# Kernel tuning notes

Measured on AMD Instinct MI355X. Metric: run time of the kernel, lower is better.

Reference implementation:

```python
import jax, jax.numpy as jnp
import numpy as np

N_CLASSES = 4
N_STEPS = 10
THRESHOLD = 0.7
ALPHA = 2.0


def _make_kernel_bias(n_classes, threshold):
    cross = np.zeros((3, 3, 3), dtype=np.float32)
    cross[1, 1, :] = 1.0
    cross[1, :, 1] = 1.0
    cross[:, 1, 1] = 1.0
    # depthwise kernel, OIDHW with I = 1 (groups = n_classes)
    kernel = (1.0 / 7.0 / (1.0 - threshold)) * np.tile(cross[None, None], (n_classes, 1, 1, 1, 1))
    bias = np.full((n_classes,), -threshold / (1.0 - threshold), dtype=np.float32)
    return jnp.asarray(kernel), jnp.asarray(bias)


def setup_inputs() -> dict:
    key = jax.random.key(0)
    k1, k2, k3 = jax.random.split(key, 3)
    B, C, D, H, W = 2, N_CLASSES, 128, 128, 128
    inp = jax.random.normal(k1, (B, C, D, H, W), dtype=jnp.float32)
    target = jax.random.randint(k2, (B, D, H, W), 0, C, dtype=jnp.int64)
    weight = jax.random.uniform(k3, (B, C), dtype=jnp.float32)
    kernel, bias = _make_kernel_bias(C, THRESHOLD)
    return {"input": inp, "target": target, "weight": weight, "kernel": kernel, "bias": bias}


def _erode(op, kernel, bias, n_classes):
    y = jax.lax.conv_general_dilated(
        op, kernel, window_strides=(1, 1, 1), padding=[(1, 1)] * 3,
        dimension_numbers=("NCDHW", "OIDHW", "NCDHW"),
        feature_group_count=n_classes)
    return jnp.maximum(y + bias[None, :, None, None, None], 0.0)


def reference(input, target, weight, kernel, bias):
    C = N_CLASSES
    probs = jax.nn.softmax(input, axis=1)
    # one_hot -> [B, D, H, W, C] -> [B, C, D, H, W]
    tgt = jnp.transpose(jax.nn.one_hot(target, C, dtype=probs.dtype), (0, 4, 1, 2, 3))
    op = jnp.square(probs - tgt)
    loss_t = jnp.zeros_like(op)
    for k in range(N_STEPS):
        op = _erode(op, kernel, bias, C)
        loss_t = loss_t + (float(k + 1) ** ALPHA) * op
    loss_t = loss_t * weight[:, :, None, None, None]
    return jnp.mean(loss_t)
```

## Files before the change

kernel.cpp:

```cpp
#include <hip/hip_runtime.h>

#define DHW   (128*128*128)
#define CDHW  (4*DHW)
#define NTOT  (2*CDHW)
#define NACC  1024

#define ROW4     32
#define IN_ROWS  12
#define S1_ROWS  10
#define IN_P4    (IN_ROWS*ROW4)
#define S1_P4    (S1_ROWS*ROW4)
#define SLOT4(z) (((z)+8)&3)
#define SLOT2(z) (((z)+8)&1)


__global__ __launch_bounds__(256, 4) void fused_sm_erode2_kernel(
    const float* __restrict__ in, const int* __restrict__ tgt,
    float4* __restrict__ dst,
    const float* __restrict__ kern, const float* __restrict__ bias,
    const float* __restrict__ weight, float c1, float c2,
    double* __restrict__ accs, int* __restrict__ flagOut)
{
    __shared__ float4 lin[4 * IN_P4];
    __shared__ float4 ls1[2 * S1_P4];
    __shared__ double wsum[4];
    __shared__ int    voteArr[16];

    const int tid = threadIdx.x;
    const int x  = blockIdx.x & 7;
    const int q  = blockIdx.x >> 3;
    const int c  = q & 3;
    const int t  = x * 32 + (q >> 2);
    const int y0 = (t & 15) << 3;
    const int zb = ((t >> 4) & 7) << 4;
    const int b  = (t >> 7) & 1;
    const int bc = b * 4 + c;
    const int fid = (bc << 7) | (((t >> 4) & 7) << 4) | (t & 15);

    const float4* in4 = (const float4*)in;
    const int4*   tg4 = (const int4*)tgt;
    const size_t  chb = ((size_t)(b * 4)) << 19;
    const size_t  co0 = chb + ((size_t)c << 19);
    const size_t  co1 = chb + ((size_t)((c + 1) & 3) << 19);
    const size_t  co2 = chb + ((size_t)((c + 2) & 3) << 19);
    const size_t  co3 = chb + ((size_t)((c + 3) & 3) << 19);
    float4*       dp  = dst + ((size_t)bc << 19);
    const float wk = kern[13];
    const float bs = bias[c];

    const int col  = tid & 31;
    const int trow = tid >> 5;

    if (tid < 16) voteArr[tid] = 0;

    const int  gy0  = y0 + trow - 2;
    const bool lv0  = ((unsigned)gy0 < 128u);
    const int  off0 = (lv0 ? gy0 : 0) * 32 + col;
    const bool act1 = (tid < 128);
    const int  gy1  = y0 + trow + 6;
    const bool lv1  = act1 && ((unsigned)gy1 < 128u);
    const int  off1 = (lv1 ? gy1 : 0) * 32 + col;

    const bool  sact1 = (tid < 64);
    const int   sr  = (tid < 32) ? 0 : 9;
    const float m1  = ((unsigned)(y0 + sr - 1) < 128u) ? 1.f : 0.f;
    const int   ci1 = (sr + 1) * 32 + (tid & 31);
    const int   so1 = sr * 32 + (tid & 31);

    const float lmask = (col == 0)  ? 0.f : 1.f;
    const float rmask = (col == 31) ? 0.f : 1.f;

    const int go4 = (y0 + trow) * 32 + col;

    const float4 f4z = make_float4(0.f, 0.f, 0.f, 0.f);
    float4 A00 = f4z, A01 = f4z, A02 = f4z, A03 = f4z;
    float4 A10 = f4z, A11 = f4z, A12 = f4z, A13 = f4z;
    int4   T0 = make_int4(0,0,0,0), T1 = make_int4(0,0,0,0);
    bool   ok0 = false, ok1 = false;
    float4 s_m = f4z, s_c = f4z, s_p = f4z;
    float4 vH  = f4z;

    auto prefetch = [&](int L) {
        const bool zok = ((unsigned)L < 128u);
        ok0 = zok && lv0;
        ok1 = zok && lv1;
        if (ok0) {
            size_t o = (size_t)(L << 12) + off0;
            A00 = in4[co0 + o];
            A01 = in4[co1 + o];
            A02 = in4[co2 + o];
            A03 = in4[co3 + o];
            T0  = tg4[((size_t)b << 19) + o];
        }
        if (ok1) {
            size_t o = (size_t)(L << 12) + off1;
            A10 = in4[co0 + o];
            A11 = in4[co1 + o];
            A12 = in4[co2 + o];
            A13 = in4[co3 + o];
            T1  = tg4[((size_t)b << 19) + o];
        }
    };
    auto op_one = [&](const float4& B0, const float4& B1, const float4& B2,
                      const float4& B3, const int4& T) -> float4 {
        float4 r;
        #define OP1(K)                                                         \
        {                                                                      \
            float vc = B0.K;                                                   \
            float sm = 1.0f + __expf(B1.K - vc) + __expf(B2.K - vc)            \
                            + __expf(B3.K - vc);                               \
            float d  = __builtin_amdgcn_rcpf(sm) - ((T.K == c) ? 1.0f : 0.0f); \
            r.K = d * d;                                                       \
        }
        OP1(x) OP1(y) OP1(z) OP1(w)
        #undef OP1
        return r;
    };
    auto commit = [&](int L) {
        float4* sl = lin + SLOT4(L) * IN_P4;
        float4 v0 = f4z, v1 = f4z;
        if (ok0) v0 = op_one(A00, A01, A02, A03, T0);
        if (ok1) v1 = op_one(A10, A11, A12, A13, T1);
        sl[tid] = v0;
        if (act1) sl[256 + tid] = v1;
    };
    auto s1one = [&](const float4* pzm, const float4* pzc, const float4* pzp,
                     int ci, float ym) -> float4 {
        float4 qC = pzc[ci];
        float4 qU = pzc[ci - 32];
        float4 qD = pzc[ci + 32];
        float4 qm = pzm[ci];
        float4 qp = pzp[ci];
        float lf = __shfl_up(qC.w, 1, 64)   * lmask;
        float rt = __shfl_down(qC.x, 1, 64) * rmask;
        float4 v;
        v.x = fmaxf((qC.x + lf   + qC.y + qU.x + qD.x + qm.x + qp.x) * wk + bs, 0.f) * ym;
        v.y = fmaxf((qC.y + qC.x + qC.z + qU.y + qD.y + qm.y + qp.y) * wk + bs, 0.f) * ym;
        v.z = fmaxf((qC.z + qC.y + qC.w + qU.z + qD.z + qm.z + qp.z) * wk + bs, 0.f) * ym;
        v.w = fmaxf((qC.w + qC.z + rt   + qU.w + qD.w + qm.w + qp.w) * wk + bs, 0.f) * ym;
        return v;
    };
    auto s1_phase = [&](int z) {
        float4* o = ls1 + SLOT2(z) * S1_P4;
        float4 vnew;
        if ((unsigned)z < 128u) {
            const float4* pzm = lin + SLOT4(z - 1) * IN_P4;
            const float4* pzc = lin + SLOT4(z)     * IN_P4;
            const float4* pzp = lin + SLOT4(z + 1) * IN_P4;
            vnew = s1one(pzm, pzc, pzp, tid + 64, 1.f);
            o[tid + 32] = vnew;
            if (sact1) o[so1] = s1one(pzm, pzc, pzp, ci1, m1);
        } else {
            vnew = f4z;
            o[tid + 32] = f4z;
            if (sact1) o[so1] = f4z;
        }
        s_m = s_c; s_c = s_p; s_p = vnew;
    };

    double part = 0.0;

    prefetch(zb - 2); commit(zb - 2);
    prefetch(zb - 1); commit(zb - 1);
    prefetch(zb);     commit(zb);
    prefetch(zb + 1);
    __syncthreads();
    s1_phase(zb - 1);

    for (int L = zb + 1; L <= zb + 17; ++L) {
        commit(L);
        __syncthreads();
        const int zp = L - 3;
        if (zp >= zb && voteArr[zp - zb] != 0)
            dp[((size_t)zp << 12) + go4] = vH;
        if (L <= zb + 16) prefetch(L + 1);
        s1_phase(L - 1);
        const int zo = L - 2;
        if (zo >= zb) {
            const float4* su = ls1 + SLOT2(zo) * S1_P4;
            float4 u4 = su[tid];
            float4 d4 = su[tid + 64];
            float lf = __shfl_up(s_c.w, 1, 64)   * lmask;
            float rt = __shfl_down(s_c.x, 1, 64) * rmask;
            float4 v;
            v.x = fmaxf((s_c.x + lf    + s_c.y + u4.x + d4.x + s_m.x + s_p.x) * wk + bs, 0.f);
            v.y = fmaxf((s_c.y + s_c.x + s_c.z + u4.y + d4.y + s_m.y + s_p.y) * wk + bs, 0.f);
            v.z = fmaxf((s_c.z + s_c.y + s_c.w + u4.z + d4.z + s_m.z + s_p.z) * wk + bs, 0.f);
            v.w = fmaxf((s_c.w + s_c.z + rt    + u4.w + d4.w + s_m.w + s_p.w) * wk + bs, 0.f);
            float pl = c1 * (s_c.x + s_c.y + s_c.z + s_c.w)
                     + c2 * (v.x   + v.y   + v.z   + v.w);
            part += (double)pl;
            bool nzv = (v.x != 0.f) || (v.y != 0.f) || (v.z != 0.f) || (v.w != 0.f);
            if (__any(nzv) && (tid & 63) == 0) atomicOr(&voteArr[zo - zb], 1);
            vH = v;
        }
    }

    __syncthreads();
    if (voteArr[15] != 0) dp[((size_t)(zb + 15) << 12) + go4] = vH;

    #pragma unroll
    for (int off = 32; off > 0; off >>= 1)
        part += __shfl_down(part, off, 64);
    if ((tid & 63) == 0) wsum[tid >> 6] = part;
    __syncthreads();
    if (tid == 0) {
        int mask = 0;
        #pragma unroll
        for (int i = 0; i < 16; ++i) mask |= (voteArr[i] ? 1 : 0) << i;
        flagOut[fid] = mask;
        double tot = (wsum[0] + wsum[1] + wsum[2] + wsum[3]) * (double)weight[bc];
        accs[blockIdx.x] = tot;
    }
}

#define E4_INP4  512
#define E4_S1P4  448
#define E4_S2P4  384
#define E4_S3P4  320

__global__ __launch_bounds__(256, 2) void erode4_kernel(
    const float4* __restrict__ src, float4* __restrict__ dst,
    const float* __restrict__ kern, const float* __restrict__ bias,
    const float* __restrict__ weight,
    float c1, float c2, float c3, float c4,
    int store, double* __restrict__ accs,
    const int* __restrict__ flagIn, int* __restrict__ flagOut)
{
    __shared__ float4 lin[4 * E4_INP4];
    __shared__ float4 ls1[2 * E4_S1P4];
    __shared__ float4 ls2[2 * E4_S2P4];
    __shared__ float4 ls3[2 * E4_S3P4];
    __shared__ double wsum[4];
    __shared__ int    sf[9];
    __shared__ int    voteArr[16];
    __shared__ unsigned sAIn;

    const int tid = threadIdx.x;
    const int bid = ((blockIdx.x & 7) << 7) | (blockIdx.x >> 3);
    const int ty = bid & 15;
    const int tz = (bid >> 4) & 7;
    const int y0 = ty << 3;
    const int zb = tz << 4;
    const int bc = bid >> 7;

    if (tid < 9) {
        int dy = tid % 3 - 1, dz = tid / 3 - 1;
        int yt = ty + dy, zt = tz + dz;
        int f = 0;
        if ((unsigned)yt < 16u && (unsigned)zt < 8u)
            f = flagIn[(bc << 7) | (zt << 4) | yt];
        sf[tid] = f;
    }
    __syncthreads();

    bool abit = false;
    if (tid < 24) {
        int L = zb - 4 + tid;
        if ((unsigned)L < 128u) {
            int zi = (L >> 4) - tz + 1;
            int m  = sf[zi * 3] | sf[zi * 3 + 1] | sf[zi * 3 + 2];
            abit = (m >> (L & 15)) & 1;
        }
    }
    unsigned long long bal = __ballot(abit);
    if (tid == 0) sAIn = (unsigned)bal;
    __syncthreads();
    const unsigned aIn = sAIn;
    if (aIn == 0) { if (tid == 0) flagOut[bid] = 0; return; }

    unsigned zc = 0xFFFFFFu;
    if (zb == 0)   zc &= 0xFFFFF0u;
    if (zb == 112) zc &= 0x0FFFFFu;
    const unsigned a1 = (aIn | aIn << 1 | aIn >> 1) & zc & 0x7FFFFEu;
    const unsigned a2 = (a1  | a1  << 1 | a1  >> 1) & zc & 0x3FFFFCu;
    const unsigned a3 = (a2  | a2  << 1 | a2  >> 1) & zc & 0x1FFFF8u;
    const unsigned a4 = (a3  | a3  << 1 | a3  >> 1) & zc & 0x0FFFF0u;

    if (tid < 16) voteArr[tid] = 0;

    const int fa  = __builtin_ctz(aIn);
    const int la  = 31 - __builtin_clz(aIn);
    const int loL = zb - 4 + (fa > 2 ? fa - 2 : 0);
    const int hiL = zb - 4 + (la + 8 < 23 ? la + 8 : 23);

    const float4* sp = src + ((size_t)bc << 19);
    float4*       dp = dst + ((size_t)bc << 19);
    const float wk = kern[13];
    const float bs = bias[bc & 3];

    const int col  = tid & 31;
    const int trow = tid >> 5;
    const int g    = trow;

    const int  gy0 = y0 - 4 + trow;
    const int  gy1 = y0 + 4 + trow;
    const bool lv0 = ((unsigned)gy0 < 128u);
    const bool lv1 = ((unsigned)gy1 < 128u);
    const int  off0 = (lv0 ? gy0 : 0) * 32 + col;
    const int  off1 = (lv1 ? gy1 : 0) * 32 + col;
    const int  yd0 = ((unsigned)((gy0 >> 3) - ty + 1) < 3u) ? ((gy0 >> 3) - ty + 1) : 1;
    const int  yd1 = ((unsigned)((gy1 >> 3) - ty + 1) < 3u) ? ((gy1 >> 3) - ty + 1) : 1;

    const int   r1  = (g < 3) ? g : g + 8;
    const float ym1 = ((unsigned)(y0 - 3 + r1) < 128u) ? 1.f : 0.f;
    const int   ci1 = (r1 + 1) * 32 + col;
    const int   R2  = (g < 2) ? g : g + 8;
    const float ym2 = ((unsigned)(y0 - 2 + R2) < 128u) ? 1.f : 0.f;
    const int   ci2 = (R2 + 2) * 32 + col;
    const int   S3  = g * 9;
    const float ym3 = ((unsigned)(y0 - 1 + S3) < 128u) ? 1.f : 0.f;
    const int   ci3 = (S3 + 3) * 32 + col;

    const float lmask = (col == 0)  ? 0.f : 1.f;
    const float rmask = (col == 31) ? 0.f : 1.f;
    const int   go4  = (y0 + trow) * 32 + col;

    const float4 f4z = make_float4(0.f, 0.f, 0.f, 0.f);
    float4 pf0 = f4z, pf1 = f4z;
    float4 p1m=f4z,p1c=f4z,p1p=f4z;
    float4 p2m=f4z,p2c=f4z,p2p=f4z;
    float4 p3m=f4z,p3c=f4z,p3p=f4z;
    float4 o1m=f4z,o1c=f4z,o1p=f4z;
    float4 q1m=f4z,q1c=f4z,q1p=f4z;
    float4 q2m=f4z,q2c=f4z,q2p=f4z;
    float4 vH = f4z;
    double part = 0.0;

    auto st7 = [&](const float4& zm, const float4& cc, const float4& zp,
                   const float4& u, const float4& d, float ym) -> float4 {
        float lf = __shfl_up(cc.w, 1, 64)   * lmask;
        float rt = __shfl_down(cc.x, 1, 64) * rmask;
        float4 v;
        v.x = fmaxf((cc.x + lf   + cc.y + u.x + d.x + zm.x + zp.x) * wk + bs, 0.f) * ym;
        v.y = fmaxf((cc.y + cc.x + cc.z + u.y + d.y + zm.y + zp.y) * wk + bs, 0.f) * ym;
        v.z = fmaxf((cc.z + cc.y + cc.w + u.z + d.z + zm.z + zp.z) * wk + bs, 0.f) * ym;
        v.w = fmaxf((cc.w + cc.z + rt   + u.w + d.w + zm.w + zp.w) * wk + bs, 0.f) * ym;
        return v;
    };
    auto s1at = [&](int z, int ci, float ym) -> float4 {
        const float4* pzm = lin + SLOT4(z - 1) * E4_INP4;
        const float4* pzc = lin + SLOT4(z)     * E4_INP4;
        const float4* pzp = lin + SLOT4(z + 1) * E4_INP4;
        return st7(pzm[ci], pzc[ci], pzp[ci], pzc[ci - 32], pzc[ci + 32], ym);
    };
    auto prefetch = [&](int L) {
        pf0 = f4z; pf1 = f4z;
        if (L >= zb - 4 && L <= zb + 19 && (unsigned)L < 128u) {
            const int zi = (L >> 4) - tz + 1;
            const int sh = L & 15;
            const float4* zp = sp + ((size_t)L << 12);
            if (lv0 && ((sf[zi * 3 + yd0] >> sh) & 1)) pf0 = zp[off0];
            if (lv1 && ((sf[zi * 3 + yd1] >> sh) & 1)) pf1 = zp[off1];
        }
    };
    auto commit = [&](int L) {
        float4* sl = lin + SLOT4(L) * E4_INP4;
        sl[trow * 32 + col]       = pf0;
        sl[(trow + 8) * 32 + col] = pf1;
    };

    prefetch(loL);
    for (int L = loL; L <= hiL; ++L) {
        commit(L);
        __syncthreads();
        const int zs = L - 5;
        if (store && zs >= zb && voteArr[zs - zb] != 0)
            dp[((size_t)zs << 12) + go4] = vH;
        if (L < hiL) prefetch(L + 1);

        {
            const int z = L - 1, ib = z - (zb - 4);
            float4 vp = f4z, vo = f4z, vq = f4z;
            if ((unsigned)ib < 24u && ((a1 >> ib) & 1)) {
                vp = s1at(z, (trow + 4) * 32 + col, 1.f);
                float4* o = ls1 + SLOT2(z) * E4_S1P4;
                if (tid < 192) o[r1 * 32 + col] = s1at(z, ci1, ym1);
                if (tid < 128) vo = s1at(z, ci2, ym2);
                if (tid < 64)  vq = s1at(z, ci3, ym3);
                o[(trow + 3) * 32 + col] = vp;
                if (z >= zb && z <= zb + 15)
                    part += (double)(c1 * (vp.x + vp.y + vp.z + vp.w));
            }
            p1m = p1c; p1c = p1p; p1p = vp;
            o1m = o1c; o1c = o1p; o1p = vo;
            q1m = q1c; q1c = q1p; q1p = vq;
        }
        {
            const int z = L - 2, ib = z - (zb - 4);
            float4 vp = f4z, vq = f4z;
            if ((unsigned)ib < 24u && ((a2 >> ib) & 1)) {
                const bool l1 = ((a1 >> ib) & 1);
                const float4* s1p_ = ls1 + SLOT2(z) * E4_S1P4;
                float4 u = l1 ? s1p_[(trow + 2) * 32 + col] : f4z;
                float4 d = l1 ? s1p_[(trow + 4) * 32 + col] : f4z;
                vp = st7(p1m, p1c, p1p, u, d, 1.f);
                float4* o = ls2 + SLOT2(z) * E4_S2P4;
                if (tid < 128) {
                    float4 u2 = l1 ? s1p_[R2 * 32 + col]       : f4z;
                    float4 d2 = l1 ? s1p_[(R2 + 2) * 32 + col] : f4z;
                    o[R2 * 32 + col] = st7(o1m, o1c, o1p, u2, d2, ym2);
                }
                if (tid < 64) {
                    float4 u3 = l1 ? s1p_[(S3 + 1) * 32 + col] : f4z;
                    float4 d3 = l1 ? s1p_[(S3 + 3) * 32 + col] : f4z;
                    vq = st7(q1m, q1c, q1p, u3, d3, ym3);
                }
                o[(trow + 2) * 32 + col] = vp;
                if (z >= zb && z <= zb + 15)
                    part += (double)(c2 * (vp.x + vp.y + vp.z + vp.w));
            }
            p2m = p2c; p2c = p2p; p2p = vp;
            q2m = q2c; q2c = q2p; q2p = vq;
        }
        {
            const int z = L - 3, ib = z - (zb - 4);
            float4 vp = f4z;
            if ((unsigned)ib < 24u && ((a3 >> ib) & 1)) {
                const bool l2 = ((a2 >> ib) & 1);
                const float4* s2p_ = ls2 + SLOT2(z) * E4_S2P4;
                float4 u = l2 ? s2p_[(trow + 1) * 32 + col] : f4z;
                float4 d = l2 ? s2p_[(trow + 3) * 32 + col] : f4z;
                vp = st7(p2m, p2c, p2p, u, d, 1.f);
                float4* o = ls3 + SLOT2(z) * E4_S3P4;
                if (tid < 64) {
                    float4 u3 = l2 ? s2p_[S3 * 32 + col]       : f4z;
                    float4 d3 = l2 ? s2p_[(S3 + 2) * 32 + col] : f4z;
                    o[S3 * 32 + col] = st7(q2m, q2c, q2p, u3, d3, ym3);
                }
                o[(trow + 1) * 32 + col] = vp;
                if (z >= zb && z <= zb + 15)
                    part += (double)(c3 * (vp.x + vp.y + vp.z + vp.w));
            }
            p3m = p3c; p3c = p3p; p3p = vp;
        }
        {
            const int z = L - 4, ib = z - (zb - 4);
            float4 v = f4z;
            if ((unsigned)ib < 24u && ((a4 >> ib) & 1)) {
                const bool l3 = ((a3 >> ib) & 1);
                const float4* s3p_ = ls3 + SLOT2(z) * E4_S3P4;
                float4 u = l3 ? s3p_[trow * 32 + col]       : f4z;
                float4 d = l3 ? s3p_[(trow + 2) * 32 + col] : f4z;
                v = st7(p3m, p3c, p3p, u, d, 1.f);
                part += (double)(c4 * (v.x + v.y + v.z + v.w));
                bool nzv = (v.x != 0.f) || (v.y != 0.f) || (v.z != 0.f) || (v.w != 0.f);
                if (__any(nzv) && (tid & 63) == 0) atomicOr(&voteArr[z - zb], 1);
            }
            vH = v;
        }
    }

    __syncthreads();
    {
        const int hp = hiL - 4;
        if (store && hp >= zb && voteArr[hp - zb] != 0)
            dp[((size_t)hp << 12) + go4] = vH;
    }

    #pragma unroll
    for (int off = 32; off > 0; off >>= 1)
        part += __shfl_down(part, off, 64);
    if ((tid & 63) == 0) wsum[tid >> 6] = part;
    __syncthreads();
    if (tid == 0) {
        int mask = 0;
        #pragma unroll
        for (int i = 0; i < 16; ++i) mask |= (voteArr[i] ? 1 : 0) << i;
        flagOut[bid] = mask;
        double tot = (wsum[0] + wsum[1] + wsum[2] + wsum[3]) * (double)weight[bc];
        atomicAdd(&accs[bid], tot);
    }
}

__global__ __launch_bounds__(1024) void finalize_kernel(
    const double* __restrict__ accs, float* __restrict__ out)
{
    __shared__ double wsum[16];
    double v = accs[threadIdx.x];
    #pragma unroll
    for (int off = 32; off > 0; off >>= 1)
        v += __shfl_down(v, off, 64);
    int lane = threadIdx.x & 63;
    int wid  = threadIdx.x >> 6;
    if (lane == 0) wsum[wid] = v;
    __syncthreads();
    if (threadIdx.x == 0) {
        double tot = 0.0;
        #pragma unroll
        for (int i = 0; i < 16; ++i) tot += wsum[i];
        out[0] = (float)(tot / (double)NTOT);
    }
}

extern "C" void kernel_launch(void* const* d_in, const int* in_sizes, int n_in,
                              void* d_out, int out_size, void* d_ws, size_t ws_size,
                              hipStream_t stream) {
    const float* in     = (const float*)d_in[0];
    const int*   tgt    = (const int*)d_in[1];
    const float* weight = (const float*)d_in[2];
    const float* kern   = (const float*)d_in[3];
    const float* bias   = (const float*)d_in[4];
    float* out = (float*)d_out;

    char* ws = (char*)d_ws;
    float*  buf0   = (float*)ws;
    float*  buf1   = (float*)(ws + (size_t)NTOT * sizeof(float));
    double* accs   = (double*)(ws + (size_t)NTOT * 2 * sizeof(float));
    int*    flagsA = (int*)(ws + (size_t)NTOT * 2 * sizeof(float) + NACC * sizeof(double));
    int*    flagsB = flagsA + NACC;

    fused_sm_erode2_kernel<<<1024, 256, 0, stream>>>(
        in, tgt, (float4*)buf0, kern, bias, weight, 1.0f, 4.0f, accs, flagsA);

    erode4_kernel<<<1024, 256, 0, stream>>>(
        (const float4*)buf0, (float4*)buf1, kern, bias, weight,
        9.0f, 16.0f, 25.0f, 36.0f, 1, accs, flagsA, flagsB);

    erode4_kernel<<<1024, 256, 0, stream>>>(
        (const float4*)buf1, (float4*)buf0, kern, bias, weight,
        49.0f, 64.0f, 81.0f, 100.0f, 0, accs, flagsB, flagsA);

    finalize_kernel<<<1, 1024, 0, stream>>>(accs, out);
}
```

Before: 150.5 us.

## Compact active tiles into a worklist and run persistent erode blocks

Result: slower. 160.5 us (+6.7%).

```diff
diff --git a/kernel.cpp b/kernel.cpp
--- a/kernel.cpp
+++ b/kernel.cpp
@@ -214,6 +214,32 @@
     }
 }
 
+__global__ __launch_bounds__(1024) void wl_build_kernel(
+    const int* __restrict__ flagIn, int* __restrict__ flagOut,
+    int* __restrict__ wl, int* __restrict__ popc)
+{
+    const int t = threadIdx.x;
+    flagOut[t] = 0;
+    if (t == 0) { wl[0] = 0; popc[0] = 0; }
+    __syncthreads();
+
+    const int ty = t & 15, tz = (t >> 4) & 7, bc = t >> 7;
+    int act = 0;
+    #pragma unroll
+    for (int dz = -1; dz <= 1; ++dz) {
+        int zt = tz + dz;
+        if ((unsigned)zt >= 8u) continue;
+        int need = (dz < 0) ? 0xF000 : (dz > 0) ? 0x000F : 0xFFFF;
+        #pragma unroll
+        for (int dy = -1; dy <= 1; ++dy) {
+            int yt = ty + dy;
+            if ((unsigned)yt >= 16u) continue;
+            act |= flagIn[(bc << 7) | (zt << 4) | yt] & need;
+        }
+    }
+    if (act) { int i = atomicAdd(&wl[0], 1); wl[1 + i] = t; }
+}
+
 #define E4_INP4  512
 #define E4_S1P4  448
 #define E4_S2P4  384
@@ -225,7 +251,8 @@
     const float* __restrict__ weight,
     float c1, float c2, float c3, float c4,
     int store, double* __restrict__ accs,
-    const int* __restrict__ flagIn, int* __restrict__ flagOut)
+    const int* __restrict__ flagIn, int* __restrict__ flagOut,
+    const int* __restrict__ wl, int* __restrict__ popc)
 {
     __shared__ float4 lin[4 * E4_INP4];
     __shared__ float4 ls1[2 * E4_S1P4];
@@ -235,241 +262,256 @@
     __shared__ int    sf[9];
     __shared__ int    voteArr[16];
     __shared__ unsigned sAIn;
-
-    const int tid = threadIdx.x;
-    const int bid = ((blockIdx.x & 7) << 7) | (blockIdx.x >> 3);
-    const int ty = bid & 15;
-    const int tz = (bid >> 4) & 7;
-    const int y0 = ty << 3;
-    const int zb = tz << 4;
-    const int bc = bid >> 7;
-
-    if (tid < 9) {
-        int dy = tid % 3 - 1, dz = tid / 3 - 1;
-        int yt = ty + dy, zt = tz + dz;
-        int f = 0;
-        if ((unsigned)yt < 16u && (unsigned)zt < 8u)
-            f = flagIn[(bc << 7) | (zt << 4) | yt];
-        sf[tid] = f;
-    }
-    __syncthreads();
-
-    bool abit = false;
-    if (tid < 24) {
-        int L = zb - 4 + tid;
-        if ((unsigned)L < 128u) {
-            int zi = (L >> 4) - tz + 1;
-            int m  = sf[zi * 3] | sf[zi * 3 + 1] | sf[zi * 3 + 2];
-            abit = (m >> (L & 15)) & 1;
-        }
-    }
-    unsigned long long bal = __ballot(abit);
-    if (tid == 0) sAIn = (unsigned)bal;
-    __syncthreads();
-    const unsigned aIn = sAIn;
-    if (aIn == 0) { if (tid == 0) flagOut[bid] = 0; return; }
-
-    unsigned zc = 0xFFFFFFu;
-    if (zb == 0)   zc &= 0xFFFFF0u;
-    if (zb == 112) zc &= 0x0FFFFFu;
-    const unsigned a1 = (aIn | aIn << 1 | aIn >> 1) & zc & 0x7FFFFEu;
-    const unsigned a2 = (a1  | a1  << 1 | a1  >> 1) & zc & 0x3FFFFCu;
-    const unsigned a3 = (a2  | a2  << 1 | a2  >> 1) & zc & 0x1FFFF8u;
-    const unsigned a4 = (a3  | a3  << 1 | a3  >> 1) & zc & 0x0FFFF0u;
-
-    if (tid < 16) voteArr[tid] = 0;
-
-    const int fa  = __builtin_ctz(aIn);
-    const int la  = 31 - __builtin_clz(aIn);
-    const int loL = zb - 4 + (fa > 2 ? fa - 2 : 0);
-    const int hiL = zb - 4 + (la + 8 < 23 ? la + 8 : 23);
-
-    const float4* sp = src + ((size_t)bc << 19);
-    float4*       dp = dst + ((size_t)bc << 19);
-    const float wk = kern[13];
-    const float bs = bias[bc & 3];
-
+    __shared__ int    sTile;
+
+    const int tid  = threadIdx.x;
+    const int cnt  = wl[0];
     const int col  = tid & 31;
     const int trow = tid >> 5;
     const int g    = trow;
-
-    const int  gy0 = y0 - 4 + trow;
-    const int  gy1 = y0 + 4 + trow;
-    const bool lv0 = ((unsigned)gy0 < 128u);
-    const bool lv1 = ((unsigned)gy1 < 128u);
-    const int  off0 = (lv0 ? gy0 : 0) * 32 + col;
-    const int  off1 = (lv1 ? gy1 : 0) * 32 + col;
-    const int  yd0 = ((unsigned)((gy0 >> 3) - ty + 1) < 3u) ? ((gy0 >> 3) - ty + 1) : 1;
-    const int  yd1 = ((unsigned)((gy1 >> 3) - ty + 1) < 3u) ? ((gy1 >> 3) - ty + 1) : 1;
-
-    const int   r1  = (g < 3) ? g : g + 8;
-    const float ym1 = ((unsigned)(y0 - 3 + r1) < 128u) ? 1.f : 0.f;
-    const int   ci1 = (r1 + 1) * 32 + col;
-    const int   R2  = (g < 2) ? g : g + 8;
-    const float ym2 = ((unsigned)(y0 - 2 + R2) < 128u) ? 1.f : 0.f;
-    const int   ci2 = (R2 + 2) * 32 + col;
-    const int   S3  = g * 9;
-    const float ym3 = ((unsigned)(y0 - 1 + S3) < 128u) ? 1.f : 0.f;
-    const int   ci3 = (S3 + 3) * 32 + col;
-
+    const float wk = kern[13];
     const float lmask = (col == 0)  ? 0.f : 1.f;
     const float rmask = (col == 31) ? 0.f : 1.f;
-    const int   go4  = (y0 + trow) * 32 + col;
-
     const float4 f4z = make_float4(0.f, 0.f, 0.f, 0.f);
-    float4 pf0 = f4z, pf1 = f4z;
-    float4 p1m=f4z,p1c=f4z,p1p=f4z;
-    float4 p2m=f4z,p2c=f4z,p2p=f4z;
-    float4 p3m=f4z,p3c=f4z,p3p=f4z;
-    float4 o1m=f4z,o1c=f4z,o1p=f4z;
-    float4 q1m=f4z,q1c=f4z,q1p=f4z;
-    float4 q2m=f4z,q2c=f4z,q2p=f4z;
-    float4 vH = f4z;
-    double part = 0.0;
-
-    auto st7 = [&](const float4& zm, const float4& cc, const float4& zp,
-                   const float4& u, const float4& d, float ym) -> float4 {
-        float lf = __shfl_up(cc.w, 1, 64)   * lmask;
-        float rt = __shfl_down(cc.x, 1, 64) * rmask;
-        float4 v;
-        v.x = fmaxf((cc.x + lf   + cc.y + u.x + d.x + zm.x + zp.x) * wk + bs, 0.f) * ym;
-        v.y = fmaxf((cc.y + cc.x + cc.z + u.y + d.y + zm.y + zp.y) * wk + bs, 0.f) * ym;
-        v.z = fmaxf((cc.z + cc.y + cc.w + u.z + d.z + zm.z + zp.z) * wk + bs, 0.f) * ym;
-        v.w = fmaxf((cc.w + cc.z + rt   + u.w + d.w + zm.w + zp.w) * wk + bs, 0.f) * ym;
-        return v;
-    };
-    auto s1at = [&](int z, int ci, float ym) -> float4 {
-        const float4* pzm = lin + SLOT4(z - 1) * E4_INP4;
-        const float4* pzc = lin + SLOT4(z)     * E4_INP4;
-        const float4* pzp = lin + SLOT4(z + 1) * E4_INP4;
-        return st7(pzm[ci], pzc[ci], pzp[ci], pzc[ci - 32], pzc[ci + 32], ym);
-    };
-    auto prefetch = [&](int L) {
-        pf0 = f4z; pf1 = f4z;
-        if (L >= zb - 4 && L <= zb + 19 && (unsigned)L < 128u) {
-            const int zi = (L >> 4) - tz + 1;
-            const int sh = L & 15;
-            const float4* zp = sp + ((size_t)L << 12);
-            if (lv0 && ((sf[zi * 3 + yd0] >> sh) & 1)) pf0 = zp[off0];
-            if (lv1 && ((sf[zi * 3 + yd1] >> sh) & 1)) pf1 = zp[off1];
-        }
-    };
-    auto commit = [&](int L) {
-        float4* sl = lin + SLOT4(L) * E4_INP4;
-        sl[trow * 32 + col]       = pf0;
-        sl[(trow + 8) * 32 + col] = pf1;
-    };
-
-    prefetch(loL);
-    for (int L = loL; L <= hiL; ++L) {
-        commit(L);
-        __syncthreads();
-        const int zs = L - 5;
-        if (store && zs >= zb && voteArr[zs - zb] != 0)
-            dp[((size_t)zs << 12) + go4] = vH;
-        if (L < hiL) prefetch(L + 1);
-
+
+    for (;;) {
+        if (tid == 0) {
+            int i = atomicAdd(popc, 1);
+            sTile = (i < cnt) ? wl[1 + i] : -1;
+        }
+        __syncthreads();
+        const int tile = sTile;
+        __syncthreads();
+        if (tile < 0) break;
+
+        const int ty = tile & 15;
+        const int tz = (tile >> 4) & 7;
+        const int y0 = ty << 3;
+        const int zb = tz << 4;
+        const int bc = tile >> 7;
+
+        if (tid < 9) {
+            int dy = tid % 3 - 1, dz = tid / 3 - 1;
+            int yt = ty + dy, zt = tz + dz;
+            int f = 0;
+            if ((unsigned)yt < 16u && (unsigned)zt < 8u)
+                f = flagIn[(bc << 7) | (zt << 4) | yt];
+            sf[tid] = f;
+        }
+        __syncthreads();
+
+        bool abit = false;
+        if (tid < 24) {
+            int L = zb - 4 + tid;
+            if ((unsigned)L < 128u) {
+                int zi = (L >> 4) - tz + 1;
+                int m  = sf[zi * 3] | sf[zi * 3 + 1] | sf[zi * 3 + 2];
+                abit = (m >> (L & 15)) & 1;
+            }
+        }
+        unsigned long long bal = __ballot(abit);
+        if (tid == 0) sAIn = (unsigned)bal;
+        __syncthreads();
+        const unsigned aIn = sAIn;
+        if (aIn == 0) continue;
+
+        unsigned zc = 0xFFFFFFu;
+        if (zb == 0)   zc &= 0xFFFFF0u;
+        if (zb == 112) zc &= 0x0FFFFFu;
+        const unsigned a1 = (aIn | aIn << 1 | aIn >> 1) & zc & 0x7FFFFEu;
+        const unsigned a2 = (a1  | a1  << 1 | a1  >> 1) & zc & 0x3FFFFCu;
+        const unsigned a3 = (a2  | a2  << 1 | a2  >> 1) & zc & 0x1FFFF8u;
+        const unsigned a4 = (a3  | a3  << 1 | a3  >> 1) & zc & 0x0FFFF0u;
+
+        if (tid < 16) voteArr[tid] = 0;
+
+        const int fa  = __builtin_ctz(aIn);
+        const int la  = 31 - __builtin_clz(aIn);
+        const int loL = zb - 4 + (fa > 2 ? fa - 2 : 0);
+        const int hiL = zb - 4 + (la + 8 < 23 ? la + 8 : 23);
+
+        const float4* sp = src + ((size_t)bc << 19);
+        float4*       dp = dst + ((size_t)bc << 19);
+        const float bs = bias[bc & 3];
+
+        const int  gy0 = y0 - 4 + trow;
+        const int  gy1 = y0 + 4 + trow;
+        const bool lv0 = ((unsigned)gy0 < 128u);
+        const bool lv1 = ((unsigned)gy1 < 128u);
+        const int  off0 = (lv0 ? gy0 : 0) * 32 + col;
+        const int  off1 = (lv1 ? gy1 : 0) * 32 + col;
+        const int  yd0 = ((unsigned)((gy0 >> 3) - ty + 1) < 3u) ? ((gy0 >> 3) - ty + 1) : 1;
+        const int  yd1 = ((unsigned)((gy1 >> 3) - ty + 1) < 3u) ? ((gy1 >> 3) - ty + 1) : 1;
+
+        const int   r1  = (g < 3) ? g : g + 8;
+        const float ym1 = ((unsigned)(y0 - 3 + r1) < 128u) ? 1.f : 0.f;
+        const int   ci1 = (r1 + 1) * 32 + col;
+        const int   R2  = (g < 2) ? g : g + 8;
+        const float ym2 = ((unsigned)(y0 - 2 + R2) < 128u) ? 1.f : 0.f;
+        const int   ci2 = (R2 + 2) * 32 + col;
+        const int   S3  = g * 9;
+        const float ym3 = ((unsigned)(y0 - 1 + S3) < 128u) ? 1.f : 0.f;
+        const int   ci3 = (S3 + 3) * 32 + col;
+
+        const int go4 = (y0 + trow) * 32 + col;
+
+        float4 pf0 = f4z, pf1 = f4z;
+        float4 p1m=f4z,p1c=f4z,p1p=f4z;
+        float4 p2m=f4z,p2c=f4z,p2p=f4z;
+        float4 p3m=f4z,p3c=f4z,p3p=f4z;
+        float4 o1m=f4z,o1c=f4z,o1p=f4z;
+        float4 q1m=f4z,q1c=f4z,q1p=f4z;
+        float4 q2m=f4z,q2c=f4z,q2p=f4z;
+        float4 vH = f4z;
+        double part = 0.0;
+
+        auto st7 = [&](const float4& zm, const float4& cc, const float4& zp,
+                       const float4& u, const float4& d, float ym) -> float4 {
+            float lf = __shfl_up(cc.w, 1, 64)   * lmask;
+            float rt = __shfl_down(cc.x, 1, 64) * rmask;
+            float4 v;
+            v.x = fmaxf((cc.x + lf   + cc.y + u.x + d.x + zm.x + zp.x) * wk + bs, 0.f) * ym;
+            v.y = fmaxf((cc.y + cc.x + cc.z + u.y + d.y + zm.y + zp.y) * wk + bs, 0.f) * ym;
+            v.z = fmaxf((cc.z + cc.y + cc.w + u.z + d.z + zm.z + zp.z) * wk + bs, 0.f) * ym;
+            v.w = fmaxf((cc.w + cc.z + rt   + u.w + d.w + zm.w + zp.w) * wk + bs, 0.f) * ym;
+            return v;
+        };
+        auto s1at = [&](int z, int ci, float ym) -> float4 {
+            const float4* pzm = lin + SLOT4(z - 1) * E4_INP4;
+            const float4* pzc = lin + SLOT4(z)     * E4_INP4;
+            const float4* pzp = lin + SLOT4(z + 1) * E4_INP4;
+            return st7(pzm[ci], pzc[ci], pzp[ci], pzc[ci - 32], pzc[ci + 32], ym);
+        };
+        auto prefetch = [&](int L) {
+            pf0 = f4z; pf1 = f4z;
+            if (L >= zb - 4 && L <= zb + 19 && (unsigned)L < 128u) {
+                const int zi = (L >> 4) - tz + 1;
+                const int sh = L & 15;
+                const float4* zp = sp + ((size_t)L << 12);
+                if (lv0 && ((sf[zi * 3 + yd0] >> sh) & 1)) pf0 = zp[off0];
+                if (lv1 && ((sf[zi * 3 + yd1] >> sh) & 1)) pf1 = zp[off1];
+            }
+        };
+        auto commit = [&](int L) {
+            float4* sl = lin + SLOT4(L) * E4_INP4;
+            sl[trow * 32 + col]       = pf0;
+            sl[(trow + 8) * 32 + col] = pf1;
+        };
+
+        prefetch(loL);
+        for (int L = loL; L <= hiL; ++L) {
+            commit(L);
+            __syncthreads();
+            const int zs = L - 5;
+            if (store && zs >= zb && voteArr[zs - zb] != 0)
+                dp[((size_t)zs << 12) + go4] = vH;
+            if (L < hiL) prefetch(L + 1);
+
+            {
+                const int z = L - 1, ib = z - (zb - 4);
+                float4 vp = f4z, vo = f4z, vq = f4z;
+                if ((unsigned)ib < 24u && ((a1 >> ib) & 1)) {
+                    vp = s1at(z, (trow + 4) * 32 + col, 1.f);
+                    float4* o = ls1 + SLOT2(z) * E4_S1P4;
+                    if (tid < 192) o[r1 * 32 + col] = s1at(z, ci1, ym1);
+                    if (tid < 128) vo = s1at(z, ci2, ym2);
+                    if (tid < 64)  vq = s1at(z, ci3, ym3);
+                    o[(trow + 3) * 32 + col] = vp;
+                    if (z >= zb && z <= zb + 15)
+                        part += (double)(c1 * (vp.x + vp.y + vp.z + vp.w));
+                }
+                p1m = p1c; p1c = p1p; p1p = vp;
+                o1m = o1c; o1c = o1p; o1p = vo;
+                q1m = q1c; q1c = q1p; q1p = vq;
+            }
+            {
+                const int z = L - 2, ib = z - (zb - 4);
+                float4 vp = f4z, vq = f4z;
+                if ((unsigned)ib < 24u && ((a2 >> ib) & 1)) {
+                    const bool l1 = ((a1 >> ib) & 1);
+                    const float4* s1p_ = ls1 + SLOT2(z) * E4_S1P4;
+                    float4 u = l1 ? s1p_[(trow + 2) * 32 + col] : f4z;
+                    float4 d = l1 ? s1p_[(trow + 4) * 32 + col] : f4z;
+                    vp = st7(p1m, p1c, p1p, u, d, 1.f);
+                    float4* o = ls2 + SLOT2(z) * E4_S2P4;
+                    if (tid < 128) {
+                        float4 u2 = l1 ? s1p_[R2 * 32 + col]       : f4z;
+                        float4 d2 = l1 ? s1p_[(R2 + 2) * 32 + col] : f4z;
+                        o[R2 * 32 + col] = st7(o1m, o1c, o1p, u2, d2, ym2);
+                    }
+                    if (tid < 64) {
+                        float4 u3 = l1 ? s1p_[(S3 + 1) * 32 + col] : f4z;
+                        float4 d3 = l1 ? s1p_[(S3 + 3) * 32 + col] : f4z;
+                        vq = st7(q1m, q1c, q1p, u3, d3, ym3);
+                    }
+                    o[(trow + 2) * 32 + col] = vp;
+                    if (z >= zb && z <= zb + 15)
+                        part += (double)(c2 * (vp.x + vp.y + vp.z + vp.w));
+                }
+                p2m = p2c; p2c = p2p; p2p = vp;
+                q2m = q2c; q2c = q2p; q2p = vq;
+            }
+            {
+                const int z = L - 3, ib = z - (zb - 4);
+                float4 vp = f4z;
+                if ((unsigned)ib < 24u && ((a3 >> ib) & 1)) {
+                    const bool l2 = ((a2 >> ib) & 1);
+                    const float4* s2p_ = ls2 + SLOT2(z) * E4_S2P4;
+                    float4 u = l2 ? s2p_[(trow + 1) * 32 + col] : f4z;
+                    float4 d = l2 ? s2p_[(trow + 3) * 32 + col] : f4z;
+                    vp = st7(p2m, p2c, p2p, u, d, 1.f);
+                    float4* o = ls3 + SLOT2(z) * E4_S3P4;
+                    if (tid < 64) {
+                        float4 u3 = l2 ? s2p_[S3 * 32 + col]       : f4z;
+                        float4 d3 = l2 ? s2p_[(S3 + 2) * 32 + col] : f4z;
+                        o[S3 * 32 + col] = st7(q2m, q2c, q2p, u3, d3, ym3);
+                    }
+                    o[(trow + 1) * 32 + col] = vp;
+                    if (z >= zb && z <= zb + 15)
+                        part += (double)(c3 * (vp.x + vp.y + vp.z + vp.w));
+                }
+                p3m = p3c; p3c = p3p; p3p = vp;
+            }
+            {
+                const int z = L - 4, ib = z - (zb - 4);
+                float4 v = f4z;
+                if ((unsigned)ib < 24u && ((a4 >> ib) & 1)) {
+                    const bool l3 = ((a3 >> ib) & 1);
+                    const float4* s3p_ = ls3 + SLOT2(z) * E4_S3P4;
+                    float4 u = l3 ? s3p_[trow * 32 + col]       : f4z;
+                    float4 d = l3 ? s3p_[(trow + 2) * 32 + col] : f4z;
+                    v = st7(p3m, p3c, p3p, u, d, 1.f);
+                    part += (double)(c4 * (v.x + v.y + v.z + v.w));
+                    bool nzv = (v.x != 0.f) || (v.y != 0.f) ||
+                               (v.z != 0.f) || (v.w != 0.f);
+                    if (__any(nzv) && (tid & 63) == 0)
+                        atomicOr(&voteArr[z - zb], 1);
+                }
+                vH = v;
+            }
+        }
+
+        __syncthreads();
         {
-            const int z = L - 1, ib = z - (zb - 4);
-            float4 vp = f4z, vo = f4z, vq = f4z;
-            if ((unsigned)ib < 24u && ((a1 >> ib) & 1)) {
-                vp = s1at(z, (trow + 4) * 32 + col, 1.f);
-                float4* o = ls1 + SLOT2(z) * E4_S1P4;
-                if (tid < 192) o[r1 * 32 + col] = s1at(z, ci1, ym1);
-                if (tid < 128) vo = s1at(z, ci2, ym2);
-                if (tid < 64)  vq = s1at(z, ci3, ym3);
-                o[(trow + 3) * 32 + col] = vp;
-                if (z >= zb && z <= zb + 15)
-                    part += (double)(c1 * (vp.x + vp.y + vp.z + vp.w));
-            }
-            p1m = p1c; p1c = p1p; p1p = vp;
-            o1m = o1c; o1c = o1p; o1p = vo;
-            q1m = q1c; q1c = q1p; q1p = vq;
-        }
-        {
-            const int z = L - 2, ib = z - (zb - 4);
-            float4 vp = f4z, vq = f4z;
-            if ((unsigned)ib < 24u && ((a2 >> ib) & 1)) {
-                const bool l1 = ((a1 >> ib) & 1);
-                const float4* s1p_ = ls1 + SLOT2(z) * E4_S1P4;
-                float4 u = l1 ? s1p_[(trow + 2) * 32 + col] : f4z;
-                float4 d = l1 ? s1p_[(trow + 4) * 32 + col] : f4z;
-                vp = st7(p1m, p1c, p1p, u, d, 1.f);
-                float4* o = ls2 + SLOT2(z) * E4_S2P4;
-                if (tid < 128) {
-                    float4 u2 = l1 ? s1p_[R2 * 32 + col]       : f4z;
-                    float4 d2 = l1 ? s1p_[(R2 + 2) * 32 + col] : f4z;
-                    o[R2 * 32 + col] = st7(o1m, o1c, o1p, u2, d2, ym2);
-                }
-                if (tid < 64) {
-                    float4 u3 = l1 ? s1p_[(S3 + 1) * 32 + col] : f4z;
-                    float4 d3 = l1 ? s1p_[(S3 + 3) * 32 + col] : f4z;
-                    vq = st7(q1m, q1c, q1p, u3, d3, ym3);
-                }
-                o[(trow + 2) * 32 + col] = vp;
-                if (z >= zb && z <= zb + 15)
-                    part += (double)(c2 * (vp.x + vp.y + vp.z + vp.w));
-            }
-            p2m = p2c; p2c = p2p; p2p = vp;
-            q2m = q2c; q2c = q2p; q2p = vq;
-        }
-        {
-            const int z = L - 3, ib = z - (zb - 4);
-            float4 vp = f4z;
-            if ((unsigned)ib < 24u && ((a3 >> ib) & 1)) {
-                const bool l2 = ((a2 >> ib) & 1);
-                const float4* s2p_ = ls2 + SLOT2(z) * E4_S2P4;
-                float4 u = l2 ? s2p_[(trow + 1) * 32 + col] : f4z;
-                float4 d = l2 ? s2p_[(trow + 3) * 32 + col] : f4z;
-                vp = st7(p2m, p2c, p2p, u, d, 1.f);
-                float4* o = ls3 + SLOT2(z) * E4_S3P4;
-                if (tid < 64) {
-                    float4 u3 = l2 ? s2p_[S3 * 32 + col]       : f4z;
-                    float4 d3 = l2 ? s2p_[(S3 + 2) * 32 + col] : f4z;
-                    o[S3 * 32 + col] = st7(q2m, q2c, q2p, u3, d3, ym3);
-                }
-                o[(trow + 1) * 32 + col] = vp;
-                if (z >= zb && z <= zb + 15)
-                    part += (double)(c3 * (vp.x + vp.y + vp.z + vp.w));
-            }
-            p3m = p3c; p3c = p3p; p3p = vp;
-        }
-        {
-            const int z = L - 4, ib = z - (zb - 4);
-            float4 v = f4z;
-            if ((unsigned)ib < 24u && ((a4 >> ib) & 1)) {
-                const bool l3 = ((a3 >> ib) & 1);
-                const float4* s3p_ = ls3 + SLOT2(z) * E4_S3P4;
-                float4 u = l3 ? s3p_[trow * 32 + col]       : f4z;
-                float4 d = l3 ? s3p_[(trow + 2) * 32 + col] : f4z;
-                v = st7(p3m, p3c, p3p, u, d, 1.f);
-                part += (double)(c4 * (v.x + v.y + v.z + v.w));
-                bool nzv = (v.x != 0.f) || (v.y != 0.f) || (v.z != 0.f) || (v.w != 0.f);
-                if (__any(nzv) && (tid & 63) == 0) atomicOr(&voteArr[z - zb], 1);
-            }
-            vH = v;
-        }
-    }
-
-    __syncthreads();
-    {
-        const int hp = hiL - 4;
-        if (store && hp >= zb && voteArr[hp - zb] != 0)
-            dp[((size_t)hp << 12) + go4] = vH;
-    }
-
-    #pragma unroll
-    for (int off = 32; off > 0; off >>= 1)
-        part += __shfl_down(part, off, 64);
-    if ((tid & 63) == 0) wsum[tid >> 6] = part;
-    __syncthreads();
-    if (tid == 0) {
-        int mask = 0;
+            const int hp = hiL - 4;
+            if (store && hp >= zb && voteArr[hp - zb] != 0)
+                dp[((size_t)hp << 12) + go4] = vH;
+        }
+
         #pragma unroll
-        for (int i = 0; i < 16; ++i) mask |= (voteArr[i] ? 1 : 0) << i;
-        flagOut[bid] = mask;
-        double tot = (wsum[0] + wsum[1] + wsum[2] + wsum[3]) * (double)weight[bc];
-        atomicAdd(&accs[bid], tot);
+        for (int off = 32; off > 0; off >>= 1)
+            part += __shfl_down(part, off, 64);
+        if ((tid & 63) == 0) wsum[tid >> 6] = part;
+        __syncthreads();
+        if (tid == 0) {
+            int mask = 0;
+            #pragma unroll
+            for (int i = 0; i < 16; ++i) mask |= (voteArr[i] ? 1 : 0) << i;
+            flagOut[tile] = mask;
+            double tot = (wsum[0] + wsum[1] + wsum[2] + wsum[3]) * (double)weight[bc];
+            atomicAdd(&accs[tile], tot);
+        }
+        __syncthreads();
     }
 }
 
@@ -508,18 +550,26 @@
     float*  buf1   = (float*)(ws + (size_t)NTOT * sizeof(float));
     double* accs   = (double*)(ws + (size_t)NTOT * 2 * sizeof(float));
     int*    flagsA = (int*)(ws + (size_t)NTOT * 2 * sizeof(float) + NACC * sizeof(double));
-    int*    flagsB = flagsA + NACC;
+    int*    flagsB = flagsA + 1024;
+    int*    wlA    = flagsB + 1024;
+    int*    popA   = wlA + 1056;
+    int*    wlB    = popA + 32;
+    int*    popB   = wlB + 1056;
 
     fused_sm_erode2_kernel<<<1024, 256, 0, stream>>>(
         in, tgt, (float4*)buf0, kern, bias, weight, 1.0f, 4.0f, accs, flagsA);
 
-    erode4_kernel<<<1024, 256, 0, stream>>>(
+    wl_build_kernel<<<1, 1024, 0, stream>>>(flagsA, flagsB, wlA, popA);
+
+    erode4_kernel<<<256, 256, 0, stream>>>(
         (const float4*)buf0, (float4*)buf1, kern, bias, weight,
-        9.0f, 16.0f, 25.0f, 36.0f, 1, accs, flagsA, flagsB);
-
-    erode4_kernel<<<1024, 256, 0, stream>>>(
+        9.0f, 16.0f, 25.0f, 36.0f, 1, accs, flagsA, flagsB, wlA, popA);
+
+    wl_build_kernel<<<1, 1024, 0, stream>>>(flagsB, flagsA, wlB, popB);
+
+    erode4_kernel<<<256, 256, 0, stream>>>(
         (const float4*)buf1, (float4*)buf0, kern, bias, weight,
-        49.0f, 64.0f, 81.0f, 100.0f, 0, accs, flagsB, flagsA);
+        49.0f, 64.0f, 81.0f, 100.0f, 0, accs, flagsB, flagsA, wlB, popB);
 
     finalize_kernel<<<1, 1024, 0, stream>>>(accs, out);
 }
```
